# Kernel optimization log

Hardware: AMD Instinct MI355X
Metric: run time of the kernel (lower is better)

Reference implementation:

```python
import jax, jax.numpy as jnp
import numpy as np

HW = 128  # BEV heatmap size hardcoded in the module

def conv2d(x, w, b, pad):
    y = jax.lax.conv_general_dilated(x, w, (1, 1), [(pad, pad), (pad, pad)],
                                     dimension_numbers=('NCHW', 'OIHW', 'NCHW'))
    return y + b[None, :, None, None]

def setup_inputs() -> dict:
    key = jax.random.key(0)
    ks = jax.random.split(key, 8)
    B, C, N = 4, 64, 4096
    middle_feat_lidar = jax.random.normal(ks[0], (B, C, HW, HW), dtype=jnp.float32)
    voxels_feat_radar = jax.random.normal(ks[1], (N, C), dtype=jnp.float32)
    rcoors = jax.random.randint(ks[2], (N, 4), 0, HW, dtype=jnp.int64)
    rcoors = rcoors.at[:, 0].set(rcoors[:, 0] % B)  # batch index in [0, B)
    rcs = jax.random.uniform(ks[3], (N,), dtype=jnp.float32) * 6.0
    gamma = jnp.array(1.0, dtype=jnp.float32)  # self.rcs_gamma
    # rcs_att: Conv2d(2, C, 1); compress: Conv2d(2C, C, 3, pad=1)
    att_w = jax.random.normal(ks[4], (C, 2, 1, 1), dtype=jnp.float32) * 0.5
    att_b = jnp.zeros((C,), dtype=jnp.float32)
    comp_w = jax.random.normal(ks[5], (C, 2 * C, 3, 3), dtype=jnp.float32) * (1.0 / np.sqrt(2 * C * 9))
    comp_b = jnp.zeros((C,), dtype=jnp.float32)
    return {"middle_feat_lidar": middle_feat_lidar, "voxels_feat_radar": voxels_feat_radar,
            "rcoors": rcoors, "batch_size": B, "rcs": rcs, "gamma": gamma,
            "att_w": att_w, "att_b": att_b, "comp_w": comp_w, "comp_b": comp_b}

def _draw_maps(rcoors, rcs, gamma, batch_size):
    # Vectorized CenterPoint-style gaussian scatter-max over all N points.
    true_rcs = jax.nn.relu(rcs)                      # (N,)
    r = jnp.floor(gamma * true_rcs + 1.0)            # int() truncation; radius >= 1
    sigma = (2.0 * r + 1.0) / 6.0                    # sigma = diameter / 6
    b = rcoors[:, 0]
    y = rcoors[:, 2].astype(jnp.float32)
    x = rcoors[:, 3].astype(jnp.float32)
    grid = jnp.arange(HW, dtype=jnp.float32)
    dy = grid[None, :] - y[:, None]                  # (N, HW) rows
    dx = grid[None, :] - x[:, None]                  # (N, HW) cols
    g = jnp.exp(-(dy[:, :, None] ** 2 + dx[:, None, :] ** 2)
                / (2.0 * sigma[:, None, None] ** 2))  # (N, HW, HW)
    eps = jnp.finfo(jnp.float32).eps
    g = jnp.where(g < eps, 0.0, g)                   # gaussian_2d eps cutoff (max is 1 at center)
    # truncate gaussian to its (2r+1) box, as the slicing in draw_heatmap_gaussian does
    box = (jnp.abs(dy[:, :, None]) <= r[:, None, None]) & (jnp.abs(dx[:, None, :]) <= r[:, None, None])
    g = jnp.where(box, g, 0.0)
    heatmap = jnp.maximum(jax.ops.segment_max(g, b, num_segments=batch_size), 0.0)          # (B,HW,HW)
    heatmap_feat = jnp.maximum(
        jax.ops.segment_max(g * true_rcs[:, None, None], b, num_segments=batch_size), 0.0)  # (B,HW,HW)
    return heatmap, heatmap_feat

def reference(middle_feat_lidar, voxels_feat_radar, rcoors, batch_size, rcs,
              gamma, att_w, att_b, comp_w, comp_b):
    heatmap, heatmap_feat = _draw_maps(rcoors, rcs, gamma, batch_size)
    hm2 = jnp.stack([heatmap, heatmap_feat], axis=1)        # (B,2,HW,HW)
    rcs_features = conv2d(hm2, att_w, att_b, pad=0)          # 1x1 conv
    fused = jnp.concatenate([middle_feat_lidar, rcs_features], axis=1)
    return conv2d(fused, comp_w, comp_b, pad=1)              # 3x3 conv
```

## Files before the change

kernel.cpp:

```cpp
#include <hip/hip_runtime.h>
#include <math.h>

#define HW 128
#define CCH 64
#define EPSF 1.1920929e-7f

typedef unsigned short u16;
typedef __attribute__((ext_vector_type(8))) short bf16x8;
typedef __attribute__((ext_vector_type(4))) float f32x4;

static __device__ __forceinline__ u16 f2bf(float x) {
    unsigned int u = __float_as_uint(x);
    unsigned int r = (u + 0x7FFFu + ((u >> 16) & 1u)) >> 16;
    return (u16)r;
}

__global__ void prep_kernel(const float* __restrict__ comp_w,
                            const float* __restrict__ att_w,
                            const float* __restrict__ att_b,
                            u16* __restrict__ Wp) {
    __shared__ float part[27][8];
    __shared__ float W3[27];
    int co = blockIdx.x, tid = threadIdx.x;
    if (tid < 216) {
        int d = tid >> 3, s = tid & 7;
        int t = d / 3, a = d - t * 3;
        float sum = 0.f;
#pragma unroll
        for (int q = 0; q < 8; ++q) {
            int c2 = s * 8 + q;
            float ww = comp_w[((size_t)co * 128 + 64 + c2) * 9 + t];
            float av = (a == 0) ? att_w[c2 * 2 + 0]
                     : (a == 1) ? att_w[c2 * 2 + 1]
                                : att_b[c2];
            sum = fmaf(ww, av, sum);
        }
        part[d][s] = sum;
    }
    __syncthreads();
    if (tid < 27) {
        float s = 0.f;
#pragma unroll
        for (int q = 0; q < 8; ++q) s += part[tid][q];
        W3[tid] = s;
    }
    __syncthreads();
    for (int k = tid; k < 672; k += 256) {
        int oct = k >> 3, j = k & 7;
        u16 v = 0;
        if (oct < 81) {
            int t = oct / 9, o = oct - t * 9;
            int ci = o * 8 + j;
            float w = 0.0f;
            if (ci < 64)      w = comp_w[((size_t)co * 128 + ci) * 9 + t];
            else if (ci < 67) w = W3[t * 3 + (ci - 64)];
            v = f2bf(w);
        }
        Wp[co * 672 + k] = v;
    }
}

__global__ __launch_bounds__(256)
void conv_kernel(const float* __restrict__ middle,
                 const int* __restrict__ rcoors,
                 const float* __restrict__ rcs,
                 const float* __restrict__ gamma_p,
                 const u16* __restrict__ Wp, const float* __restrict__ comp_b,
                 float* __restrict__ out, int N) {
    const int bx = blockIdx.x, by = blockIdx.y, b = blockIdx.z;
    const int tid = threadIdx.x;
    const int wave = tid >> 6, lane = tid & 63;
    const int col = lane & 15, quad = lane >> 4;
    const int i0 = by * 16 - 1, j0 = bx * 16 - 1;

    __shared__ u16 Xs[18 * 18 * 72];
    __shared__ int   VP[4096];
    __shared__ float VI[4096];
    __shared__ float VT[4096];
    __shared__ int nv;

    if (tid == 0) nv = 0;
    __syncthreads();

    {
        float gam = gamma_p[0];
        for (int n = tid; n < N; n += 256) {
            int4 rc = ((const int4*)rcoors)[n];
            if (rc.x != b) continue;
            float tr = fmaxf(rcs[n], 0.0f);
            float r = floorf(gam * tr + 1.0f);
            int ri = (int)r;
            int yi = rc.z, xi = rc.w;
            if (yi + ri < i0 || yi - ri > i0 + 17 ||
                xi + ri < j0 || xi - ri > j0 + 17) continue;
            float sigma = (2.0f * r + 1.0f) * (1.0f / 6.0f);
            float inv2s2 = 1.0f / (2.0f * sigma * sigma);
            int slot = atomicAdd(&nv, 1);
            if (slot < 4096) {
                VP[slot] = yi | (xi << 8) | (ri << 16);
                VI[slot] = inv2s2;
                VT[slot] = tr;
            }
        }
    }
    __syncthreads();
    const int nvl = min(nv, 4096);

    {
        const float* midB = middle + (size_t)b * CCH * HW * HW;
        for (int u = tid; u < 324 * 9; u += 256) {
            int oct = u / 324, site = u - oct * 324;
            int rr = site / 18, cc = site - rr * 18;
            int gi = i0 + rr, gj = j0 + cc;
            bool in = ((unsigned)gi < HW) && ((unsigned)gj < HW);
            union { u16 h[8]; uint4 v; } pk;
            pk.v = make_uint4(0u, 0u, 0u, 0u);
            if (in) {
                if (oct < 8) {
                    const float* p = midB + (size_t)oct * 8 * HW * HW + gi * HW + gj;
#pragma unroll
                    for (int j = 0; j < 8; ++j)
                        pk.h[j] = f2bf(p[(size_t)j * HW * HW]);
                } else {
                    float Hv = 0.0f, Fv = 0.0f;
                    for (int v = 0; v < nvl; ++v) {
                        int pv = VP[v];
                        int dy = gi - (pv & 0xFF);
                        int dx = gj - ((pv >> 8) & 0xFF);
                        int ri = pv >> 16;
                        if (abs(dy) > ri || abs(dx) > ri) continue;
                        float g = expf(-(float)(dy * dy + dx * dx) * VI[v]);
                        if (g < EPSF) continue;
                        Hv = fmaxf(Hv, g);
                        Fv = fmaxf(Fv, g * VT[v]);
                    }
                    pk.h[0] = f2bf(Hv);
                    pk.h[1] = f2bf(Fv);
                    pk.h[2] = 0x3F80u;
                }
            }
            *(uint4*)(Xs + site * 72 + oct * 8) = pk.v;
        }
    }
    __syncthreads();

    f32x4 acc[4][4];
#pragma unroll
    for (int m = 0; m < 4; ++m)
#pragma unroll
        for (int n = 0; n < 4; ++n) acc[m][n] = (f32x4){0.f, 0.f, 0.f, 0.f};

#pragma unroll
    for (int c = 0; c < 21; ++c) {
        bf16x8 af[4];
#pragma unroll
        for (int m = 0; m < 4; ++m)
            af[m] = *(const bf16x8*)(Wp + (m * 16 + col) * 672 + c * 32 + quad * 8);

        int oct = c * 4 + quad;
        if (oct > 80) oct = 80;
        int t  = oct / 9;
        int o  = oct - t * 9;
        int dy = t / 3, dx = t - dy * 3;
        const u16* Bb = Xs + ((wave * 4 + dy) * 18 + (col + dx)) * 72 + o * 8;

        bf16x8 bfr[4];
#pragma unroll
        for (int n = 0; n < 4; ++n)
            bfr[n] = *(const bf16x8*)(Bb + n * (18 * 72));

#pragma unroll
        for (int m = 0; m < 4; ++m)
#pragma unroll
            for (int n = 0; n < 4; ++n)
                acc[m][n] = __builtin_amdgcn_mfma_f32_16x16x32_bf16(af[m], bfr[n], acc[m][n], 0, 0, 0);
    }

#pragma unroll
    for (int m = 0; m < 4; ++m) {
        int co0 = m * 16 + quad * 4;
#pragma unroll
        for (int n = 0; n < 4; ++n) {
            int i = by * 16 + wave * 4 + n;
            int j = bx * 16 + col;
            float* o0 = out + (((size_t)(b * 64 + co0) * HW + i) * HW + j);
#pragma unroll
            for (int r = 0; r < 4; ++r)
                o0[(size_t)r * HW * HW] = acc[m][n][r] + comp_b[co0 + r];
        }
    }
}

extern "C" void kernel_launch(void* const* d_in, const int* in_sizes, int n_in,
                              void* d_out, int out_size, void* d_ws, size_t ws_size,
                              hipStream_t stream) {
    const float* middle  = (const float*)d_in[0];
    const int*   rcoors  = (const int*)d_in[2];
    const float* rcs     = (const float*)d_in[4];
    const float* gamma   = (const float*)d_in[5];
    const float* att_w   = (const float*)d_in[6];
    const float* att_b   = (const float*)d_in[7];
    const float* comp_w  = (const float*)d_in[8];
    const float* comp_b  = (const float*)d_in[9];
    float* out = (float*)d_out;

    int B = in_sizes[0] / (CCH * HW * HW);
    int N = in_sizes[4];

    u16* Wp = (u16*)d_ws;

    prep_kernel<<<dim3(64), 256, 0, stream>>>(comp_w, att_w, att_b, Wp);
    conv_kernel<<<dim3(8, 8, B), 256, 0, stream>>>(middle, rcoors, rcs, gamma,
                                                   Wp, comp_b, out, N);
}
```

Measured before the change: 124.0 us.

## Shrink conv tiles to 4x16 rows and scatter gaussians via shared atomicMax

Each block now covers 4 output rows instead of 16, so the grid has four times as many blocks. The output channels are split across the waves, one 16-channel slice per wave, which cuts per-thread accumulators and lets launch bounds ask for 4 blocks per CU. The heatmap is no longer a gather over a point list in shared memory. Each matching point scatters its truncated gaussian box into a small shared buffer with float atomicMax, which drops the big VP/VI/VT arrays and the per-site loop over every point. In exchange, every block rescans all N points for its smaller tile and loads more halo rows overall, and the atomicMax relies on the values being non-negative so their bit patterns order correctly.

```diff
diff --git a/kernel.cpp b/kernel.cpp
--- a/kernel.cpp
+++ b/kernel.cpp
@@ -60,7 +60,7 @@
     }
 }
 
-__global__ __launch_bounds__(256)
+__global__ __launch_bounds__(256, 4)
 void conv_kernel(const float* __restrict__ middle,
                  const int* __restrict__ rcoors,
                  const float* __restrict__ rcs,
@@ -71,15 +71,12 @@
     const int tid = threadIdx.x;
     const int wave = tid >> 6, lane = tid & 63;
     const int col = lane & 15, quad = lane >> 4;
-    const int i0 = by * 16 - 1, j0 = bx * 16 - 1;
-
-    __shared__ u16 Xs[18 * 18 * 72];
-    __shared__ int   VP[4096];
-    __shared__ float VI[4096];
-    __shared__ float VT[4096];
-    __shared__ int nv;
-
-    if (tid == 0) nv = 0;
+    const int i0 = by * 4 - 1, j0 = bx * 16 - 1;
+
+    __shared__ u16 Xs[6 * 18 * 72];
+    __shared__ float HF[108 * 2];
+
+    if (tid < 216) HF[tid] = 0.0f;
     __syncthreads();
 
     {
@@ -91,102 +88,97 @@
             float r = floorf(gam * tr + 1.0f);
             int ri = (int)r;
             int yi = rc.z, xi = rc.w;
-            if (yi + ri < i0 || yi - ri > i0 + 17 ||
+            if (yi + ri < i0 || yi - ri > i0 + 5 ||
                 xi + ri < j0 || xi - ri > j0 + 17) continue;
             float sigma = (2.0f * r + 1.0f) * (1.0f / 6.0f);
             float inv2s2 = 1.0f / (2.0f * sigma * sigma);
-            int slot = atomicAdd(&nv, 1);
-            if (slot < 4096) {
-                VP[slot] = yi | (xi << 8) | (ri << 16);
-                VI[slot] = inv2s2;
-                VT[slot] = tr;
+            int ylo = max(max(yi - ri, i0), 0);
+            int yhi = min(min(yi + ri, i0 + 5), HW - 1);
+            int xlo = max(max(xi - ri, j0), 0);
+            int xhi = min(min(xi + ri, j0 + 17), HW - 1);
+            for (int iy = ylo; iy <= yhi; ++iy) {
+                float dy = (float)(iy - yi);
+                for (int ix = xlo; ix <= xhi; ++ix) {
+                    float dx = (float)(ix - xi);
+                    float g = expf(-(dy * dy + dx * dx) * inv2s2);
+                    if (g < EPSF) continue;
+                    int st = (iy - i0) * 18 + (ix - j0);
+                    atomicMax((int*)&HF[st * 2 + 0], __float_as_int(g));
+                    float gf = g * tr;
+                    if (gf > 0.0f)
+                        atomicMax((int*)&HF[st * 2 + 1], __float_as_int(gf));
+                }
             }
         }
     }
-    __syncthreads();
-    const int nvl = min(nv, 4096);
 
     {
         const float* midB = middle + (size_t)b * CCH * HW * HW;
-        for (int u = tid; u < 324 * 9; u += 256) {
-            int oct = u / 324, site = u - oct * 324;
+        for (int u = tid; u < 108 * 8; u += 256) {
+            int oct = u / 108, site = u - oct * 108;
             int rr = site / 18, cc = site - rr * 18;
             int gi = i0 + rr, gj = j0 + cc;
             bool in = ((unsigned)gi < HW) && ((unsigned)gj < HW);
             union { u16 h[8]; uint4 v; } pk;
             pk.v = make_uint4(0u, 0u, 0u, 0u);
             if (in) {
-                if (oct < 8) {
-                    const float* p = midB + (size_t)oct * 8 * HW * HW + gi * HW + gj;
-#pragma unroll
-                    for (int j = 0; j < 8; ++j)
-                        pk.h[j] = f2bf(p[(size_t)j * HW * HW]);
-                } else {
-                    float Hv = 0.0f, Fv = 0.0f;
-                    for (int v = 0; v < nvl; ++v) {
-                        int pv = VP[v];
-                        int dy = gi - (pv & 0xFF);
-                        int dx = gj - ((pv >> 8) & 0xFF);
-                        int ri = pv >> 16;
-                        if (abs(dy) > ri || abs(dx) > ri) continue;
-                        float g = expf(-(float)(dy * dy + dx * dx) * VI[v]);
-                        if (g < EPSF) continue;
-                        Hv = fmaxf(Hv, g);
-                        Fv = fmaxf(Fv, g * VT[v]);
-                    }
-                    pk.h[0] = f2bf(Hv);
-                    pk.h[1] = f2bf(Fv);
-                    pk.h[2] = 0x3F80u;
-                }
+                const float* p = midB + (size_t)oct * 8 * HW * HW + gi * HW + gj;
+#pragma unroll
+                for (int j = 0; j < 8; ++j)
+                    pk.h[j] = f2bf(p[(size_t)j * HW * HW]);
             }
             *(uint4*)(Xs + site * 72 + oct * 8) = pk.v;
         }
     }
     __syncthreads();
 
-    f32x4 acc[4][4];
-#pragma unroll
-    for (int m = 0; m < 4; ++m)
-#pragma unroll
-        for (int n = 0; n < 4; ++n) acc[m][n] = (f32x4){0.f, 0.f, 0.f, 0.f};
+    if (tid < 108) {
+        int site = tid;
+        int rr = site / 18, cc = site - rr * 18;
+        int gi = i0 + rr, gj = j0 + cc;
+        union { u16 h[8]; uint4 v; } pk;
+        pk.v = make_uint4(0u, 0u, 0u, 0u);
+        if (((unsigned)gi < HW) && ((unsigned)gj < HW)) {
+            pk.h[0] = f2bf(HF[site * 2 + 0]);
+            pk.h[1] = f2bf(HF[site * 2 + 1]);
+            pk.h[2] = 0x3F80u;
+        }
+        *(uint4*)(Xs + site * 72 + 8 * 8) = pk.v;
+    }
+    __syncthreads();
+
+    f32x4 acc[4];
+#pragma unroll
+    for (int n = 0; n < 4; ++n) acc[n] = (f32x4){0.f, 0.f, 0.f, 0.f};
 
 #pragma unroll
     for (int c = 0; c < 21; ++c) {
-        bf16x8 af[4];
-#pragma unroll
-        for (int m = 0; m < 4; ++m)
-            af[m] = *(const bf16x8*)(Wp + (m * 16 + col) * 672 + c * 32 + quad * 8);
+        bf16x8 af = *(const bf16x8*)(Wp + (wave * 16 + col) * 672 + c * 32 + quad * 8);
 
         int oct = c * 4 + quad;
         if (oct > 80) oct = 80;
         int t  = oct / 9;
         int o  = oct - t * 9;
         int dy = t / 3, dx = t - dy * 3;
-        const u16* Bb = Xs + ((wave * 4 + dy) * 18 + (col + dx)) * 72 + o * 8;
-
-        bf16x8 bfr[4];
-#pragma unroll
-        for (int n = 0; n < 4; ++n)
-            bfr[n] = *(const bf16x8*)(Bb + n * (18 * 72));
-
-#pragma unroll
-        for (int m = 0; m < 4; ++m)
-#pragma unroll
-            for (int n = 0; n < 4; ++n)
-                acc[m][n] = __builtin_amdgcn_mfma_f32_16x16x32_bf16(af[m], bfr[n], acc[m][n], 0, 0, 0);
-    }
-
-#pragma unroll
-    for (int m = 0; m < 4; ++m) {
-        int co0 = m * 16 + quad * 4;
+        const u16* Bb = Xs + (dy * 18 + (col + dx)) * 72 + o * 8;
+
 #pragma unroll
         for (int n = 0; n < 4; ++n) {
-            int i = by * 16 + wave * 4 + n;
-            int j = bx * 16 + col;
+            bf16x8 bfr = *(const bf16x8*)(Bb + n * (18 * 72));
+            acc[n] = __builtin_amdgcn_mfma_f32_16x16x32_bf16(af, bfr, acc[n], 0, 0, 0);
+        }
+    }
+
+    {
+        int co0 = wave * 16 + quad * 4;
+        int j = bx * 16 + col;
+#pragma unroll
+        for (int n = 0; n < 4; ++n) {
+            int i = by * 4 + n;
             float* o0 = out + (((size_t)(b * 64 + co0) * HW + i) * HW + j);
 #pragma unroll
             for (int r = 0; r < 4; ++r)
-                o0[(size_t)r * HW * HW] = acc[m][n][r] + comp_b[co0 + r];
+                o0[(size_t)r * HW * HW] = acc[n][r] + comp_b[co0 + r];
         }
     }
 }
@@ -210,6 +202,6 @@
     u16* Wp = (u16*)d_ws;
 
     prep_kernel<<<dim3(64), 256, 0, stream>>>(comp_w, att_w, att_b, Wp);
-    conv_kernel<<<dim3(8, 8, B), 256, 0, stream>>>(middle, rcoors, rcs, gamma,
-                                                   Wp, comp_b, out, N);
-}
+    conv_kernel<<<dim3(8, 32, B), 256, 0, stream>>>(middle, rcoors, rcs, gamma,
+                                                    Wp, comp_b, out, N);
+}
```

After: 147.1 us. +18.6%, slower.
